# Performance work log

Measured on AMD Instinct MI355X. Metric: run time of the kernel, lower is better.

## Reference

```python
import jax, jax.numpy as jnp
import numpy as np
from jax import lax

B, S, H, T = 64, 512, 768, 9


def setup_inputs() -> dict:
    key = jax.random.key(0)
    ks = jax.random.split(key, 7)
    hidden = jax.random.normal(ks[0], (B, S, H), dtype=jnp.float32)
    W = jax.random.normal(ks[1], (H, T), dtype=jnp.float32) * 0.02
    b = jax.random.normal(ks[2], (T,), dtype=jnp.float32) * 0.02
    start_trans = jax.random.normal(ks[3], (T,), dtype=jnp.float32) * 0.1
    end_trans = jax.random.normal(ks[4], (T,), dtype=jnp.float32) * 0.1
    trans = jax.random.normal(ks[5], (T, T), dtype=jnp.float32) * 0.1
    labels = jax.random.randint(ks[6], (B, S), 0, T, dtype=jnp.int64)
    return {"hidden": hidden, "W": W, "b": b, "start_trans": start_trans,
            "end_trans": end_trans, "trans": trans, "labels": labels}


def _crf_nll(emissions, labels, start_trans, end_trans, trans):
    # emissions: [B,S,T], labels: [B,S] int. mask = labels > -1 (torchcrf semantics).
    maskf = (labels > -1).astype(emissions.dtype)          # [B,S]
    tags = jnp.maximum(labels, 0)                          # safe indexing

    # ---- numerator: score of the gold path ----
    tags0 = tags[:, 0]                                     # [B]
    num0 = start_trans[tags0] + jnp.take_along_axis(emissions[:, 0], tags0[:, None], axis=1)[:, 0]

    em_t = jnp.swapaxes(emissions[:, 1:], 0, 1)            # [S-1,B,T]
    tg_t = jnp.swapaxes(tags[:, 1:], 0, 1)                 # [S-1,B]
    mk_t = jnp.swapaxes(maskf[:, 1:], 0, 1)                # [S-1,B]

    def num_step(carry, xs):
        score, prev = carry
        em, tg, mk = xs
        step = trans[prev, tg] + jnp.take_along_axis(em, tg[:, None], axis=1)[:, 0]
        score = score + step * mk
        prev = jnp.where(mk > 0, tg, prev)
        return (score, prev), None

    (num, last_tags), _ = lax.scan(num_step, (num0, tags0), (em_t, tg_t, mk_t))
    num = num + end_trans[last_tags]                       # [B]

    # ---- denominator: log-partition via forward algorithm (log-semiring scan) ----
    alpha0 = start_trans[None, :] + emissions[:, 0]        # [B,T]

    def den_step(alpha, xs):
        em, mk = xs
        new = jax.nn.logsumexp(alpha[:, :, None] + trans[None, :, :], axis=1) + em  # [B,T]
        alpha = jnp.where(mk[:, None] > 0, new, alpha)
        return alpha, None

    alpha, _ = lax.scan(den_step, alpha0, (em_t, mk_t))
    den = jax.nn.logsumexp(alpha + end_trans[None, :], axis=1)  # [B]

    # model returns -crf(...) with reduction='mean'  =>  mean NLL
    return jnp.mean(den - num)


def reference(hidden, W, b, start_trans, end_trans, trans, labels):
    # token-classification head: [B,S,H] @ [H,T] -> emissions [B,S,T]
    emissions = jnp.einsum('bsh,ht->bst', hidden, W) + b
    return _crf_nll(emissions, labels, start_trans, end_trans, trans)
```

## Files before the change

### kernel.cpp

```cpp
#include <hip/hip_runtime.h>
#include <hip/hip_bf16.h>

constexpr int Bn = 64, Sn = 512, Hn = 768, Tn = 9;
constexpr int EMS = 12;
constexpr int CHUNKS = 32, CLEN = 16;
constexpr int WPAD = 776;

typedef __attribute__((ext_vector_type(8))) short bf16x8;
typedef __attribute__((ext_vector_type(4))) float f32x4;

__device__ __forceinline__ short f2bf(float x) {
    __hip_bfloat16 h = __float2bfloat16(x);
    return *reinterpret_cast<short*>(&h);
}

__device__ __forceinline__ float lse9(const float* e) {
    float m01 = fmaxf(e[0], e[1]), m23 = fmaxf(e[2], e[3]);
    float m45 = fmaxf(e[4], e[5]), m67 = fmaxf(e[6], e[7]);
    float m = fmaxf(fmaxf(fmaxf(m01, m23), fmaxf(m45, m67)), e[8]);
    float s = 0.f;
#pragma unroll
    for (int k = 0; k < 9; ++k) s += __expf(e[k] - m);
    return m + __logf(s);
}

__global__ __launch_bounds__(256, 2) void emis_kernel(
        const float* __restrict__ hidden, const float* __restrict__ W,
        const float* __restrict__ bias, float* __restrict__ em) {
    __shared__ float Wt[Tn * WPAD];
    const int tid = threadIdx.x, lane = tid & 63;
    for (int f = tid; f < Hn * Tn; f += 256) {
        int h = f / 9, t = f - 9 * h;
        Wt[t * WPAD + h] = W[f];
    }
    __syncthreads();

    const int c16 = lane & 15, hi = lane >> 4;
    const bool on = c16 < Tn;
    bf16x8 bfrag[24];
#pragma unroll
    for (int m = 0; m < 24; ++m) {
        bf16x8 bf;
#pragma unroll
        for (int e = 0; e < 8; ++e) {
            float w = on ? Wt[c16 * WPAD + 32 * m + hi * 8 + e] : 0.f;
            bf[e] = f2bf(w);
        }
        bfrag[m] = bf;
    }
    const float bcol = on ? bias[c16] : 0.f;

    const int wid  = blockIdx.x * 4 + (tid >> 6);
    const int row0 = wid * 16;
    const float* abase = hidden + (size_t)(row0 + c16) * Hn + hi * 8;

    f32x4 acc = {0.f, 0.f, 0.f, 0.f};
#pragma unroll
    for (int m = 0; m < 24; ++m) {
        float4 u0 = *reinterpret_cast<const float4*>(abase + 32 * m);
        float4 u1 = *reinterpret_cast<const float4*>(abase + 32 * m + 4);
        bf16x8 af;
        af[0] = f2bf(u0.x); af[1] = f2bf(u0.y); af[2] = f2bf(u0.z); af[3] = f2bf(u0.w);
        af[4] = f2bf(u1.x); af[5] = f2bf(u1.y); af[6] = f2bf(u1.z); af[7] = f2bf(u1.w);
        acc = __builtin_amdgcn_mfma_f32_16x16x32_bf16(af, bfrag[m], acc, 0, 0, 0);
    }
    if (on) {
        float* o = em + (size_t)(row0 + hi * 4) * EMS + c16;
#pragma unroll
        for (int i = 0; i < 4; ++i) o[(size_t)i * EMS] = acc[i] + bcol;
    }
}

__global__ __launch_bounds__(128) void chunk_kernel(
        const float* __restrict__ em, const float* __restrict__ trans,
        const int* __restrict__ labels, float* __restrict__ Mws) {
    const int b = blockIdx.x / CHUNKS;
    const int c = blockIdx.x % CHUNKS;
    const int tid = threadIdx.x;
    const bool act = tid < 81;
    const int i = tid / 9, j = tid % 9;
    __shared__ float Mbuf[2][9][12];
    __shared__ float emch[CLEN][EMS];
    __shared__ int   labch[CLEN];
    const int s0 = c * CLEN;
    const float* emb = em + ((size_t)b * Sn + s0) * EMS;
    for (int idx = tid; idx < CLEN * EMS; idx += 128)
        (&emch[0][0])[idx] = emb[idx];
    if (tid < CLEN) labch[tid] = labels[b * Sn + s0 + tid];
    float tc[9], row[9];
    float nv = (i == j) ? 0.f : -1e30f;
    if (act) {
#pragma unroll
        for (int k = 0; k < 9; ++k) tc[k] = trans[k * 9 + j];
#pragma unroll
        for (int k = 0; k < 9; ++k) row[k] = (k == i) ? 0.f : -1e30f;
    }
    __syncthreads();
    const int sbeg = (c == 0) ? 1 : 0;
    for (int sl = sbeg; sl < CLEN; ++sl) {
        if (act) {
            float e[9];
#pragma unroll
            for (int k = 0; k < 9; ++k) e[k] = row[k] + tc[k];
            float cand = lse9(e) + emch[sl][j];
            if (labch[sl] > -1) nv = cand;
            Mbuf[sl & 1][i][j] = nv;
        }
        __syncthreads();
        if (act) {
#pragma unroll
            for (int k = 0; k < 9; ++k) row[k] = Mbuf[sl & 1][i][k];
        }
    }
    if (act) Mws[(size_t)(b * CHUNKS + c) * 81 + tid] = nv;
}

__global__ __launch_bounds__(128) void final_kernel(
        const float* __restrict__ em, const float* __restrict__ Mws,
        const float* __restrict__ start, const float* __restrict__ endt,
        const float* __restrict__ trans, const int* __restrict__ labels,
        float* __restrict__ out) {
    const int b = blockIdx.x, tid = threadIdx.x;
    __shared__ float Ml[CHUNKS][9][12];
    __shared__ float red[128];
    for (int idx = tid; idx < CHUNKS * 81; idx += 128) {
        int c = idx / 81, r = idx % 81;
        Ml[c][r / 9][r % 9] = Mws[(size_t)(b * CHUNKS + c) * 81 + r];
    }
    const int* lb = labels + b * Sn;
    float np = 0.f;
    for (int s = tid; s < Sn; s += 128) {
        if (s >= 1) {
            int l = lb[s];
            if (l > -1) {
                int tp = lb[s - 1]; tp = tp > -1 ? tp : 0;
                np += trans[tp * 9 + l] + em[((size_t)b * Sn + s) * EMS + l];
            }
        }
    }
    red[tid] = np;
    __syncthreads();
    for (int off = 64; off > 0; off >>= 1) {
        if (tid < off) red[tid] += red[tid + off];
        __syncthreads();
    }
    if (tid < 9) {
        const int j = tid;
        float alpha[9];
#pragma unroll
        for (int k = 0; k < 9; ++k)
            alpha[k] = start[k] + em[(size_t)b * Sn * EMS + k];
        for (int c = 0; c < CHUNKS; ++c) {
            float e[9];
#pragma unroll
            for (int k = 0; k < 9; ++k) e[k] = alpha[k] + Ml[c][k][j];
            float nv = lse9(e);
#pragma unroll
            for (int k = 0; k < 9; ++k) alpha[k] = __shfl(nv, k, 64);
        }
        if (j == 0) {
            float e[9];
#pragma unroll
            for (int k = 0; k < 9; ++k) e[k] = alpha[k] + endt[k];
            float den = lse9(e);
            int t0 = lb[0] > -1 ? lb[0] : 0;
            float num = red[0] + start[t0] + em[(size_t)b * Sn * EMS + t0];
            int lt = lb[Sn - 1] > -1 ? lb[Sn - 1] : 0;
            num += endt[lt];
            atomicAdd(out, (den - num) * (1.0f / Bn));
        }
    }
}

extern "C" void kernel_launch(void* const* d_in, const int* in_sizes, int n_in,
                              void* d_out, int out_size, void* d_ws, size_t ws_size,
                              hipStream_t stream) {
    const float* hidden = (const float*)d_in[0];
    const float* W      = (const float*)d_in[1];
    const float* bias   = (const float*)d_in[2];
    const float* start  = (const float*)d_in[3];
    const float* endt   = (const float*)d_in[4];
    const float* trans  = (const float*)d_in[5];
    const int*   labels = (const int*)d_in[6];
    float* out = (float*)d_out;

    float* em  = (float*)d_ws;
    float* Mws = em + (size_t)Bn * Sn * EMS;

    hipMemsetAsync(d_out, 0, sizeof(float), stream);
    emis_kernel<<<512, 256, 0, stream>>>(hidden, W, bias, em);
    chunk_kernel<<<Bn * CHUNKS, 128, 0, stream>>>(em, trans, labels, Mws);
    final_kernel<<<Bn, 128, 0, stream>>>(em, Mws, start, endt, trans, labels, out);
}
```

Before: 201.4 us.

## Stage hidden tiles into LDS with async double-buffered swizzled loads

Rewrites the emission GEMM to copy hidden-state tiles directly from global memory into LDS with global_load_lds. It double-buffers 64-column K chunks and XOR-swizzles them to avoid bank conflicts. W fragments are pre-converted to bf16 once into shared memory instead of being held as 24 register fragments per lane. The aim is to overlap loads with MFMA work and free registers. The cost is a barrier per chunk and fewer outstanding global loads than the fully unrolled direct-load version.

```diff
diff --git a/kernel.cpp b/kernel.cpp
--- a/kernel.cpp
+++ b/kernel.cpp
@@ -4,7 +4,9 @@
 constexpr int Bn = 64, Sn = 512, Hn = 768, Tn = 9;
 constexpr int EMS = 12;
 constexpr int CHUNKS = 32, CLEN = 16;
-constexpr int WPAD = 776;
+constexpr int ROWS = 64;
+constexpr int KC = 64;
+constexpr int NKC = Hn / KC;
 
 typedef __attribute__((ext_vector_type(8))) short bf16x8;
 typedef __attribute__((ext_vector_type(4))) float f32x4;
@@ -12,6 +14,12 @@
 __device__ __forceinline__ short f2bf(float x) {
     __hip_bfloat16 h = __float2bfloat16(x);
     return *reinterpret_cast<short*>(&h);
+}
+
+__device__ __forceinline__ void gl_lds16(const void* g, void* l) {
+    __builtin_amdgcn_global_load_lds(
+        (const __attribute__((address_space(1))) void*)g,
+        (__attribute__((address_space(3))) void*)l, 16, 0, 0);
 }
 
 __device__ __forceinline__ float lse9(const float* e) {
@@ -27,47 +35,69 @@
 __global__ __launch_bounds__(256, 2) void emis_kernel(
         const float* __restrict__ hidden, const float* __restrict__ W,
         const float* __restrict__ bias, float* __restrict__ em) {
-    __shared__ float Wt[Tn * WPAD];
-    const int tid = threadIdx.x, lane = tid & 63;
-    for (int f = tid; f < Hn * Tn; f += 256) {
-        int h = f / 9, t = f - 9 * h;
-        Wt[t * WPAD + h] = W[f];
-    }
-    __syncthreads();
+    __shared__ __align__(16) float Abuf[2][ROWS * KC];
+    __shared__ __align__(16) bf16x8 Wf[24 * 4 * 16];
+
+    const int tid = threadIdx.x, lane = tid & 63, wv = tid >> 6;
+    const int R0 = blockIdx.x * ROWS;
+
+    auto stage = [&](int kc, int bufi) {
+#pragma unroll
+        for (int gg = 0; gg < 4; ++gg) {
+            const int g = wv * 4 + gg;
+            const int row = 4 * g + (lane >> 4);
+            const int cs = lane & 15;
+            const char* src = (const char*)(hidden + (size_t)(R0 + row) * Hn + kc * KC)
+                              + ((cs ^ (row & 7)) << 4);
+            gl_lds16(src, (char*)&Abuf[bufi][0] + (g << 10));
+        }
+    };
+
+    stage(0, 0);
+
+    for (int n = tid; n < 24 * 4 * 16; n += 256) {
+        const int mm = n >> 6, hj = (n >> 4) & 3, cc = n & 15;
+        bf16x8 bf;
+#pragma unroll
+        for (int e = 0; e < 8; ++e) {
+            float w = (cc < Tn) ? W[(mm * 32 + hj * 8 + e) * Tn + cc] : 0.f;
+            bf[e] = f2bf(w);
+        }
+        Wf[n] = bf;
+    }
 
     const int c16 = lane & 15, hi = lane >> 4;
     const bool on = c16 < Tn;
-    bf16x8 bfrag[24];
-#pragma unroll
-    for (int m = 0; m < 24; ++m) {
-        bf16x8 bf;
-#pragma unroll
-        for (int e = 0; e < 8; ++e) {
-            float w = on ? Wt[c16 * WPAD + 32 * m + hi * 8 + e] : 0.f;
-            bf[e] = f2bf(w);
-        }
-        bfrag[m] = bf;
-    }
     const float bcol = on ? bias[c16] : 0.f;
-
-    const int wid  = blockIdx.x * 4 + (tid >> 6);
-    const int row0 = wid * 16;
-    const float* abase = hidden + (size_t)(row0 + c16) * Hn + hi * 8;
+    const int rloc = wv * 16 + c16;
+    const int swz = rloc & 7;
+
+    __syncthreads();
 
     f32x4 acc = {0.f, 0.f, 0.f, 0.f};
-#pragma unroll
-    for (int m = 0; m < 24; ++m) {
-        float4 u0 = *reinterpret_cast<const float4*>(abase + 32 * m);
-        float4 u1 = *reinterpret_cast<const float4*>(abase + 32 * m + 4);
-        bf16x8 af;
-        af[0] = f2bf(u0.x); af[1] = f2bf(u0.y); af[2] = f2bf(u0.z); af[3] = f2bf(u0.w);
-        af[4] = f2bf(u1.x); af[5] = f2bf(u1.y); af[6] = f2bf(u1.z); af[7] = f2bf(u1.w);
-        acc = __builtin_amdgcn_mfma_f32_16x16x32_bf16(af, bfrag[m], acc, 0, 0, 0);
-    }
+    for (int kc = 0; kc < NKC; ++kc) {
+        if (kc + 1 < NKC) stage(kc + 1, (kc + 1) & 1);
+        const char* Ab = (const char*)&Abuf[kc & 1][0] + rloc * KC * 4;
+#pragma unroll
+        for (int ml = 0; ml < 2; ++ml) {
+            f32x4 a0 = *(const f32x4*)(Ab + (((ml * 8 + 2 * hi)     ^ swz) << 4));
+            f32x4 a1 = *(const f32x4*)(Ab + (((ml * 8 + 2 * hi + 1) ^ swz) << 4));
+            bf16x8 af;
+            af[0] = f2bf(a0[0]); af[1] = f2bf(a0[1]);
+            af[2] = f2bf(a0[2]); af[3] = f2bf(a0[3]);
+            af[4] = f2bf(a1[0]); af[5] = f2bf(a1[1]);
+            af[6] = f2bf(a1[2]); af[7] = f2bf(a1[3]);
+            const int mmg = kc * 2 + ml;
+            acc = __builtin_amdgcn_mfma_f32_16x16x32_bf16(
+                af, Wf[(mmg * 4 + hi) * 16 + c16], acc, 0, 0, 0);
+        }
+        __syncthreads();
+    }
+
     if (on) {
-        float* o = em + (size_t)(row0 + hi * 4) * EMS + c16;
-#pragma unroll
-        for (int i = 0; i < 4; ++i) o[(size_t)i * EMS] = acc[i] + bcol;
+#pragma unroll
+        for (int i = 0; i < 4; ++i)
+            em[(size_t)(R0 + wv * 16 + hi * 4 + i) * EMS + c16] = acc[i] + bcol;
     }
 }
 
@@ -188,7 +218,7 @@
     float* Mws = em + (size_t)Bn * Sn * EMS;
 
     hipMemsetAsync(d_out, 0, sizeof(float), stream);
-    emis_kernel<<<512, 256, 0, stream>>>(hidden, W, bias, em);
+    emis_kernel<<<Bn * Sn / ROWS, 256, 0, stream>>>(hidden, W, bias, em);
     chunk_kernel<<<Bn * CHUNKS, 128, 0, stream>>>(em, trans, labels, Mws);
     final_kernel<<<Bn, 128, 0, stream>>>(em, Mws, start, endt, trans, labels, out);
 }
```

After: 197.8 us. Within noise of the previous version (-1.7%).
